# Performance work log

Hardware: AMD Instinct MI355X
Metric: run time of the kernel (lower is better)

Reference implementation:

```python
import jax, jax.numpy as jnp
import numpy as np

T, B, E, H = 256, 8, 512, 32
EXP = 512            # number of expanded (periodic-image) keys
SMOOTH = 20.0        # smooth_factor


def setup_inputs() -> dict:
    key = jax.random.key(0)
    ks = jax.random.split(key, 12)
    s = 1.0 / np.sqrt(E)
    return {
        "query": jax.random.normal(ks[0], (T, B, E), dtype=jnp.float32),
        "outcell_index": jax.random.randint(ks[1], (B, EXP), 0, T),
        "expand_mask": jax.random.bernoulli(ks[2], 0.1, (B, EXP)),
        "key_padding_mask": jax.random.bernoulli(ks[3], 0.1, (B, T)),
        "local_attention_weight": jax.random.uniform(ks[4], (B, T, T + EXP), dtype=jnp.float32),
        "Wq": jax.random.normal(ks[5], (E, E), dtype=jnp.float32) * s,
        "bq": jnp.zeros((E,), dtype=jnp.float32),
        "Wk": jax.random.normal(ks[6], (E, E), dtype=jnp.float32) * s,   # k_bias=False
        "Wv": jax.random.normal(ks[7], (E, E), dtype=jnp.float32) * s,
        "bv": jnp.zeros((E,), dtype=jnp.float32),
        "Wo": jax.random.normal(ks[8], (E, E), dtype=jnp.float32) * s,
        "bo": jnp.zeros((E,), dtype=jnp.float32),
    }


def reference(query, outcell_index, expand_mask, key_padding_mask,
              local_attention_weight, Wq, bq, Wk, Wv, bv, Wo, bo):
    t, b, e = query.shape
    hd = e // H
    # QKV projections (torch Linear: y = x @ W.T + b)
    q = jnp.einsum('tbe,fe->tbf', query, Wq) + bq
    k = jnp.einsum('tbe,fe->tbf', query, Wk)          # no k bias
    v = jnp.einsum('tbe,fe->tbf', query, Wv) + bv
    # PBC gather-expand K/V along the time axis
    oc = outcell_index.T[:, :, None]                  # [EXP, B, 1]
    k = jnp.concatenate([k, jnp.take_along_axis(k, oc, axis=0)], axis=0)  # [S,B,E]
    v = jnp.concatenate([v, jnp.take_along_axis(v, oc, axis=0)], axis=0)
    s_len = k.shape[0]
    # [len, B, E] -> [B, H, len, hd]
    qh = q.reshape(t, b, H, hd).transpose(1, 2, 0, 3)
    kh = k.reshape(s_len, b, H, hd).transpose(1, 2, 0, 3)
    vh = v.reshape(s_len, b, H, hd).transpose(1, 2, 0, 3)
    # NOTE: forward() never applies self.scaling in this path (faithful)
    scores = jnp.einsum('bhtd,bhsd->bhts', qh, kh)    # [B,H,T,S]
    law = local_attention_weight[:, None]             # [B,1,T,S]
    scores = (scores + SMOOTH) * law - SMOOTH         # smooth softmax
    kpm = jnp.concatenate([key_padding_mask, expand_mask], axis=1)  # [B,S]
    scores = jnp.where(kpm[:, None, None, :], -jnp.inf, scores)
    probs = jax.nn.softmax(scores, axis=-1)
    probs = probs * law                               # post-softmax reweight
    attn = jnp.einsum('bhts,bhsd->bhtd', probs, vh)   # [B,H,T,hd]
    attn = attn.transpose(2, 0, 1, 3).reshape(t, b, e)
    return jnp.einsum('tbe,fe->tbf', attn, Wo) + bo
```

## Files before the change

### kernel.cpp

```cpp
#include <hip/hip_runtime.h>
#include <stdint.h>

#define T_ 256
#define B_ 8
#define E_ 512
#define H_ 32
#define HD_ 16
#define EXP_ 512
#define S_ 768
#define M_ 2048
#define SMOOTH_ 20.0f
#define PSTR 40
#define VSTR 800
#define OSTR 20
#define LOG2E_ 1.44269504f
#define MB0_  (-100.988655f)

typedef __attribute__((ext_vector_type(8)))  short bf16x8;
typedef __attribute__((ext_vector_type(4)))  float f32x4;
typedef __attribute__((ext_vector_type(16))) float f32x16;

__device__ __forceinline__ unsigned int pku(float a, float b)
{
    return ((__float_as_uint(a) + 0x8000u) >> 16) |
           ((__float_as_uint(b) + 0x8000u) & 0xFFFF0000u);
}
__device__ __forceinline__ ushort bf1(float a)
{
    unsigned int u = __float_as_uint(a);
    u = u + 0x7FFFu + ((u >> 16) & 1u);
    return (ushort)(u >> 16);
}

union U16 { uint4 u; bf16x8 v; };

template<bool AF, bool BF>
__device__ __forceinline__ void gemm_body(const void* __restrict__ Xp, int xstep,
                                          const void* __restrict__ Wp, int wstep,
                                          f32x4 acc[2][2],
                                          ushort* As, ushort* Bs)
{
    const int tid  = threadIdx.x;
    const int lrow = tid >> 2;
    const int kq   = tid & 3;
    const int l    = tid & 63;
    const int w    = tid >> 6;
    const int wm   = w & 1;
    const int wn   = w >> 1;
    const int lq   = l >> 4;
    const int ln   = l & 15;

    ushort* Aw = &As[lrow * 72 + kq * 16];
    ushort* Bw = &Bs[lrow * 72 + kq * 16];

    const float*  Xf = (const float*)Xp;
    const ushort* Xh = (const ushort*)Xp;
    const float*  Wf = (const float*)Wp;
    const ushort* Wh = (const ushort*)Wp;

    float4 fa0, fa1, fa2, fa3, fb0, fb1, fb2, fb3;
    uint4  ha0, ha1, hb0, hb1;

    if (AF) {
        fa0 = *(const float4*)&Xf[0];  fa1 = *(const float4*)&Xf[4];
        fa2 = *(const float4*)&Xf[8];  fa3 = *(const float4*)&Xf[12];
    } else {
        ha0 = *(const uint4*)&Xh[0];   ha1 = *(const uint4*)&Xh[8];
    }
    if (BF) {
        fb0 = *(const float4*)&Wf[0];  fb1 = *(const float4*)&Wf[4];
        fb2 = *(const float4*)&Wf[8];  fb3 = *(const float4*)&Wf[12];
    } else {
        hb0 = *(const uint4*)&Wh[0];   hb1 = *(const uint4*)&Wh[8];
    }

    for (int it = 0; it < E_ / 64; ++it) {
        __syncthreads();
        if (AF) {
            *(uint4*)&Aw[0] = make_uint4(pku(fa0.x, fa0.y), pku(fa0.z, fa0.w),
                                         pku(fa1.x, fa1.y), pku(fa1.z, fa1.w));
            *(uint4*)&Aw[8] = make_uint4(pku(fa2.x, fa2.y), pku(fa2.z, fa2.w),
                                         pku(fa3.x, fa3.y), pku(fa3.z, fa3.w));
        } else {
            *(uint4*)&Aw[0] = ha0;
            *(uint4*)&Aw[8] = ha1;
        }
        if (BF) {
            *(uint4*)&Bw[0] = make_uint4(pku(fb0.x, fb0.y), pku(fb0.z, fb0.w),
                                         pku(fb1.x, fb1.y), pku(fb1.z, fb1.w));
            *(uint4*)&Bw[8] = make_uint4(pku(fb2.x, fb2.y), pku(fb2.z, fb2.w),
                                         pku(fb3.x, fb3.y), pku(fb3.z, fb3.w));
        } else {
            *(uint4*)&Bw[0] = hb0;
            *(uint4*)&Bw[8] = hb1;
        }
        __syncthreads();
        if (it < E_ / 64 - 1) {
            if (AF) {
                Xf += xstep;
                fa0 = *(const float4*)&Xf[0];  fa1 = *(const float4*)&Xf[4];
                fa2 = *(const float4*)&Xf[8];  fa3 = *(const float4*)&Xf[12];
            } else {
                Xh += xstep;
                ha0 = *(const uint4*)&Xh[0];   ha1 = *(const uint4*)&Xh[8];
            }
            if (BF) {
                Wf += wstep;
                fb0 = *(const float4*)&Wf[0];  fb1 = *(const float4*)&Wf[4];
                fb2 = *(const float4*)&Wf[8];  fb3 = *(const float4*)&Wf[12];
            } else {
                Wh += wstep;
                hb0 = *(const uint4*)&Wh[0];   hb1 = *(const uint4*)&Wh[8];
            }
        }
#pragma unroll
        for (int kb = 0; kb < 2; ++kb) {
            bf16x8 af0 = *(const bf16x8*)&As[(32 * wm + ln) * 72 + 32 * kb + lq * 8];
            bf16x8 af1 = *(const bf16x8*)&As[(32 * wm + 16 + ln) * 72 + 32 * kb + lq * 8];
            bf16x8 bf0 = *(const bf16x8*)&Bs[(32 * wn + ln) * 72 + 32 * kb + lq * 8];
            bf16x8 bf1 = *(const bf16x8*)&Bs[(32 * wn + 16 + ln) * 72 + 32 * kb + lq * 8];
            acc[0][0] = __builtin_amdgcn_mfma_f32_16x16x32_bf16(af0, bf0, acc[0][0], 0, 0, 0);
            acc[0][1] = __builtin_amdgcn_mfma_f32_16x16x32_bf16(af0, bf1, acc[0][1], 0, 0, 0);
            acc[1][0] = __builtin_amdgcn_mfma_f32_16x16x32_bf16(af1, bf0, acc[1][0], 0, 0, 0);
            acc[1][1] = __builtin_amdgcn_mfma_f32_16x16x32_bf16(af1, bf1, acc[1][1], 0, 0, 0);
        }
    }
}

__global__ __launch_bounds__(256)
void qkv_gemm(const float* __restrict__ X,
              const float* __restrict__ Wq, const float* __restrict__ Wk,
              const float* __restrict__ Wv,
              const float* __restrict__ bq, const float* __restrict__ bv,
              ushort* __restrict__ Qb, ushort* __restrict__ Kb,
              ushort* __restrict__ Vb)
{
    __shared__ __align__(16) ushort AsBs[2 * 64 * 72];
    ushort* As = AsBs;
    ushort* Bs = AsBs + 64 * 72;

    const int z = blockIdx.z;
    const float* W     = (z == 0) ? Wq : (z == 1 ? Wk : Wv);
    const float* bias  = (z == 0) ? bq : (z == 2 ? bv : nullptr);
    ushort* dst        = (z == 0) ? Qb : (z == 1 ? Kb : Vb);

    const int m0 = blockIdx.y * 64;
    const int n0 = blockIdx.x * 64;

    f32x4 acc[2][2];
#pragma unroll
    for (int i = 0; i < 2; ++i)
#pragma unroll
        for (int j = 0; j < 2; ++j)
            acc[i][j] = (f32x4){0.f, 0.f, 0.f, 0.f};

    const int tid  = threadIdx.x;
    const int lrow = tid >> 2;
    const int kq   = tid & 3;
    gemm_body<true, true>(&X[(size_t)(m0 + lrow) * E_ + kq * 16], 64,
                          &W[(size_t)(n0 + lrow) * E_ + kq * 16], 64,
                          acc, As, Bs);

    const int l  = tid & 63;
    const int w  = tid >> 6;
    const int wm = w & 1;
    const int wn = w >> 1;
    const int lq = l >> 4;
    const int ln = l & 15;

    const float b0_ = bias ? bias[n0 + 32 * wn + ln]      : 0.f;
    const float b1_ = bias ? bias[n0 + 32 * wn + 16 + ln] : 0.f;

    __syncthreads();
    ushort* Ls = As;
#pragma unroll
    for (int j = 0; j < 2; ++j) {
        const float bb = j ? b1_ : b0_;
#pragma unroll
        for (int i = 0; i < 2; ++i)
#pragma unroll
            for (int r = 0; r < 4; ++r)
                Ls[(32 * wm + 16 * i + lq * 4 + r) * 72 + 32 * wn + 16 * j + ln] =
                    bf1(acc[i][j][r] + bb);
    }
    __syncthreads();

    {
        const int lm = tid & 63;
        const int hh = tid >> 6;
        uint4 f0 = *(const uint4*)&Ls[lm * 72 + hh * 16];
        uint4 f1 = *(const uint4*)&Ls[lm * 72 + hh * 16 + 8];
        const int m = m0 + lm;
        const int t = m >> 3;
        const int b = m & 7;
        const int h = (n0 >> 4) + hh;
        ushort* dp = &dst[(((size_t)(b * H_ + h)) * T_ + t) * HD_];
        *(uint4*)&dp[0] = f0;
        *(uint4*)&dp[8] = f1;
    }
}

__global__ __launch_bounds__(256)
void out_gemm(const ushort* __restrict__ Ab, const float* __restrict__ Wo,
              const float* __restrict__ bo, float* __restrict__ dst)
{
    __shared__ __align__(16) ushort AsBs[2 * 64 * 72];
    ushort* As = AsBs;
    ushort* Bs = AsBs + 64 * 72;

    const int m0 = blockIdx.y * 64;
    const int n0 = blockIdx.x * 64;

    f32x4 acc[2][2];
#pragma unroll
    for (int i = 0; i < 2; ++i)
#pragma unroll
        for (int j = 0; j < 2; ++j)
            acc[i][j] = (f32x4){0.f, 0.f, 0.f, 0.f};

    const int tid  = threadIdx.x;
    const int lrow = tid >> 2;
    const int kq   = tid & 3;
    const int m    = m0 + lrow;
    const int t    = m >> 3;
    const int b    = m & 7;
    gemm_body<false, true>(&Ab[(((size_t)(b * H_ + kq)) * T_ + t) * HD_], 4 * T_ * HD_,
                           &Wo[(size_t)(n0 + lrow) * E_ + kq * 16], 64,
                           acc, As, Bs);

    const int l  = tid & 63;
    const int w  = tid >> 6;
    const int wm = w & 1;
    const int wn = w >> 1;
    const int lq = l >> 4;
    const int ln = l & 15;

    const float bo0 = bo[n0 + 32 * wn + ln];
    const float bo1 = bo[n0 + 32 * wn + 16 + ln];

    __syncthreads();
    float* Lf = (float*)AsBs;
#pragma unroll
    for (int j = 0; j < 2; ++j) {
        const float bb = j ? bo1 : bo0;
#pragma unroll
        for (int i = 0; i < 2; ++i)
#pragma unroll
            for (int r = 0; r < 4; ++r)
                Lf[(32 * wm + 16 * i + lq * 4 + r) * 68 + 32 * wn + 16 * j + ln] =
                    acc[i][j][r] + bb;
    }
    __syncthreads();

    {
        const int lm = tid & 63;
        const int hh = tid >> 6;
        float* dp = &dst[(size_t)(m0 + lm) * E_ + n0 + hh * 16];
#pragma unroll
        for (int c = 0; c < 4; ++c) {
            float4 v = *(const float4*)&Lf[lm * 68 + hh * 16 + c * 4];
            *(float4*)&dp[c * 4] = v;
        }
    }
}

__device__ __forceinline__ void scat8(ushort* d, uint4 u)
{
    d[0 * VSTR] = (ushort)(u.x);  d[1 * VSTR] = (ushort)(u.x >> 16);
    d[2 * VSTR] = (ushort)(u.y);  d[3 * VSTR] = (ushort)(u.y >> 16);
    d[4 * VSTR] = (ushort)(u.z);  d[5 * VSTR] = (ushort)(u.z >> 16);
    d[6 * VSTR] = (ushort)(u.w);  d[7 * VSTR] = (ushort)(u.w >> 16);
}

__global__ __launch_bounds__(512)
void attn_kernel(const ushort* __restrict__ Qb, const ushort* __restrict__ Kb,
                 const ushort* __restrict__ Vb, const float* __restrict__ LAW,
                 const int* __restrict__ kpm, const int* __restrict__ em,
                 const int* __restrict__ oc, ushort* __restrict__ Ab)
{
    __shared__ __align__(16) ushort Ks[S_ * HD_];
    __shared__ __align__(16) ushort Vt[HD_ * VSTR];
    __shared__ __align__(16) float  msf[S_];
    __shared__ __align__(16) ushort Pb[8][32 * PSTR];
    __shared__ __align__(16) float  Zpart[2][128];

    float*  Obuf = (float*)Ks;
    ushort* Ob   = (ushort*)Vt;

    const int tid    = threadIdx.x;
    const int blk    = blockIdx.x;
    const int bh     = blk >> 1;
    const int thalf  = blk & 1;
    const int b      = bh >> 5;
    const int h      = bh & 31;

    ((uint4*)Ks)[tid] = ((const uint4*)&Kb[(size_t)bh * T_ * HD_])[tid];
    {
        const int t    = tid >> 1;
        const int half = tid & 1;
        uint4 v = *(const uint4*)&Vb[((size_t)bh * T_ + t) * HD_ + half * 8];
        scat8(&Vt[half * 8 * VSTR + t], v);
    }
    {
        const int j   = tid;
        const int src = oc[b * EXP_ + j];
        const uint4* kr = (const uint4*)&Kb[((size_t)bh * T_ + src) * HD_];
        *(uint4*)&Ks[(T_ + j) * HD_ + 0] = kr[0];
        *(uint4*)&Ks[(T_ + j) * HD_ + 8] = kr[1];
        const uint4* vr = (const uint4*)&Vb[((size_t)bh * T_ + src) * HD_];
        scat8(&Vt[T_ + j], vr[0]);
        scat8(&Vt[8 * VSTR + T_ + j], vr[1]);
    }
    {
        const int s = tid;
        const int m = (s < T_) ? kpm[b * T_ + s] : em[b * EXP_ + (s - T_)];
        msf[s] = m ? -1.0e5f : MB0_;
        if (tid < 256) {
            const int s2 = 512 + tid;
            msf[s2] = em[b * EXP_ + (s2 - T_)] ? -1.0e5f : MB0_;
        }
    }

    const int w      = tid >> 6;
    const int l      = tid & 63;
    const int slane  = l & 31;
    const int khalf  = l >> 5;
    const int wt     = w & 3;
    const int sh     = w >> 2;
    const int tbase  = thalf * 128 + wt * 32;
    bf16x8 qf = *(const bf16x8*)&Qb[((size_t)bh * T_ + tbase + slane) * HD_ + khalf * 8];

    __syncthreads();

    const f32x16 zero16 = {0.f,0.f,0.f,0.f,0.f,0.f,0.f,0.f,
                           0.f,0.f,0.f,0.f,0.f,0.f,0.f,0.f};
    f32x4 o0 = {0.f, 0.f, 0.f, 0.f};
    f32x4 o1 = {0.f, 0.f, 0.f, 0.f};
    float zacc[16];
#pragma unroll
    for (int r = 0; r < 16; ++r) zacc[r] = 0.f;

    const float* lawb = &LAW[((size_t)b * T_ + tbase + khalf * 4) * S_ + slane];
    ushort* pw = &Pb[w][slane];
    const int tl = l & 15;
    const int kg = l >> 4;

    for (int i = sh * 12; i < sh * 12 + 12; ++i) {
        bf16x8 kf = *(const bf16x8*)&Ks[(i * 32 + slane) * HD_ + khalf * 8];

        float lw[16];
        const float* lp = lawb + i * 32;
#pragma unroll
        for (int r = 0; r < 16; ++r)
            lw[r] = lp[(size_t)((r & 3) + 8 * (r >> 2)) * S_];

        f32x16 sc = __builtin_amdgcn_mfma_f32_32x32x16_bf16(qf, kf, zero16, 0, 0, 0);
        const float mb = msf[i * 32 + slane];

#pragma unroll
        for (int r = 0; r < 16; ++r) {
            const float lwK = lw[r] * LOG2E_;
            const float arg = __builtin_fmaf(sc[r], lwK,
                              __builtin_fmaf(lwK, SMOOTH_, mb));
            const float e = __builtin_amdgcn_exp2f(arg);
            zacc[r] += e;
            const float p = e * lw[r];
            pw[((r & 3) + 8 * (r >> 2) + 4 * khalf) * PSTR] =
                (ushort)((__float_as_uint(p) + 0x8000u) >> 16);
        }

        bf16x8 vf = *(const bf16x8*)&Vt[tl * VSTR + i * 32 + kg * 8];
        {
            const ushort* pr0 = &Pb[w][(0 * 16 + tl) * PSTR + kg * 8];
            U16 u;
            uint2 a0 = *(const uint2*)pr0;
            uint2 a1 = *(const uint2*)(pr0 + 4);
            u.u = make_uint4(a0.x, a0.y, a1.x, a1.y);
            o0 = __builtin_amdgcn_mfma_f32_16x16x32_bf16(vf, u.v, o0, 0, 0, 0);
            const ushort* pr1 = &Pb[w][(1 * 16 + tl) * PSTR + kg * 8];
            uint2 b0 = *(const uint2*)pr1;
            uint2 b1 = *(const uint2*)(pr1 + 4);
            u.u = make_uint4(b0.x, b0.y, b1.x, b1.y);
            o1 = __builtin_amdgcn_mfma_f32_16x16x32_bf16(vf, u.v, o1, 0, 0, 0);
        }
    }

#pragma unroll
    for (int m = 1; m < 32; m <<= 1) {
#pragma unroll
        for (int r = 0; r < 16; ++r)
            zacc[r] += __shfl_xor(zacc[r], m);
    }

    __syncthreads();

    if (l == 0 || l == 32) {
#pragma unroll
        for (int r = 0; r < 16; ++r)
            Zpart[sh][wt * 32 + (r & 3) + 8 * (r >> 2) + 4 * khalf] = zacc[r];
    }
    if (sh == 1) {
#pragma unroll
        for (int th = 0; th < 2; ++th) {
            const f32x4 o = th ? o1 : o0;
            *(float4*)&Obuf[((wt * 2 + th) * 16 + tl) * OSTR + kg * 4] =
                make_float4(o[0], o[1], o[2], o[3]);
        }
    }
    __syncthreads();

    if (sh == 0) {
#pragma unroll
        for (int th = 0; th < 2; ++th) {
            const int trow = wt * 32 + th * 16 + tl;
            const float Zt  = Zpart[0][trow] + Zpart[1][trow];
            const float inv = (Zt > 0.f) ? 1.f / Zt : 0.f;
            float4 po = *(const float4*)&Obuf[((wt * 2 + th) * 16 + tl) * OSTR + kg * 4];
            const f32x4 o = th ? o1 : o0;
            float ov[4] = {(o[0] + po.x) * inv, (o[1] + po.y) * inv,
                           (o[2] + po.z) * inv, (o[3] + po.w) * inv};
            *(uint*)&Ob[trow * 16 + kg * 4]     = pku(ov[0], ov[1]);
            *(uint*)&Ob[trow * 16 + kg * 4 + 2] = pku(ov[2], ov[3]);
        }
    }
    __syncthreads();

    if (tid < 256) {
        ushort* dp = &Ab[(((size_t)(b * H_ + h)) * T_ + thalf * 128) * HD_];
        *(uint4*)&dp[tid * 8] = *(const uint4*)&Ob[tid * 8];
    }
}

extern "C" void kernel_launch(void* const* d_in, const int* in_sizes, int n_in,
                              void* d_out, int out_size, void* d_ws, size_t ws_size,
                              hipStream_t stream)
{
    const float* query = (const float*)d_in[0];
    const int*   oc    = (const int*)d_in[1];
    const int*   em    = (const int*)d_in[2];
    const int*   kpm   = (const int*)d_in[3];
    const float* law   = (const float*)d_in[4];
    const float* Wq    = (const float*)d_in[5];
    const float* bq    = (const float*)d_in[6];
    const float* Wk    = (const float*)d_in[7];
    const float* Wv    = (const float*)d_in[8];
    const float* bv    = (const float*)d_in[9];
    const float* Wo    = (const float*)d_in[10];
    const float* bo    = (const float*)d_in[11];
    float* out = (float*)d_out;

    ushort* Qb = (ushort*)d_ws;
    ushort* Kb = Qb + (size_t)1048576;
    ushort* Vb = Kb + (size_t)1048576;
    ushort* Ab = Vb + (size_t)1048576;

    dim3 gq(E_ / 64, M_ / 64, 3);
    qkv_gemm<<<gq, 256, 0, stream>>>(query, Wq, Wk, Wv, bq, bv, Qb, Kb, Vb);

    attn_kernel<<<B_ * H_ * 2, 512, 0, stream>>>(Qb, Kb, Vb, law, kpm, em, oc, Ab);

    dim3 go(E_ / 64, M_ / 64, 1);
    out_gemm<<<go, 256, 0, stream>>>(Ab, Wo, bo, out);
}
```

Measured before the change: 130.8 us.

## Fuse QKV projection into attention kernel, one block per batch-head

Replaces the separate QKV GEMM and attention kernels with one kernel in which each (batch, head) block computes its own 256x48 Q/K/V slice straight from fp32 input and weights into shared memory, then runs attention. This removes the Q/K/V global round trip and one launch, and the PBC gather becomes a shared-memory copy. In exchange the grid drops from 512 to 256 blocks, each block rereads the whole query batch slice (256x512 fp32), and large shared memory limits occupancy. Each block now walks all 24 key chunks instead of splitting them across two wave groups.

Measured after the change: 138.6 us. 1.06x slower.

```diff
diff --git a/kernel.cpp b/kernel.cpp
--- a/kernel.cpp
+++ b/kernel.cpp
@@ -12,7 +12,6 @@
 #define SMOOTH_ 20.0f
 #define PSTR 40
 #define VSTR 800
-#define OSTR 20
 #define LOG2E_ 1.44269504f
 #define MB0_  (-100.988655f)
 
@@ -33,6 +32,218 @@
 }
 
 union U16 { uint4 u; bf16x8 v; };
+
+__global__ __launch_bounds__(512)
+void qkv_attn_kernel(const float* __restrict__ X,
+                     const float* __restrict__ Wq, const float* __restrict__ Wk,
+                     const float* __restrict__ Wv,
+                     const float* __restrict__ bq, const float* __restrict__ bv,
+                     const float* __restrict__ LAW,
+                     const int* __restrict__ kpm, const int* __restrict__ em,
+                     const int* __restrict__ oc, ushort* __restrict__ Ab)
+{
+    __shared__ __align__(16) char raw[82944];
+    ushort* Ks  = (ushort*)(raw);
+    ushort* Vt  = (ushort*)(raw + 24576);
+    ushort* Qi  = (ushort*)(raw + 50176);
+    float*  msf = (float*) (raw + 58368);
+    ushort* Pbb = (ushort*)(raw + 61440);
+    float*  Zb  = (float*) (raw + 81920);
+    ushort* As  = (ushort*)(raw);
+    ushort* Bs  = (ushort*)(raw + 36864);
+    ushort* Ob  = Qi;
+
+    const int bh  = blockIdx.x;
+    const int b   = bh >> 5;
+    const int h   = bh & 31;
+    const int tid = threadIdx.x;
+    const int w   = tid >> 6;
+    const int l   = tid & 63;
+
+    const int lr = tid >> 1;
+    const int kq = tid & 1;
+    const float* Xr = &X[((size_t)lr * 8 + b) * E_ + kq * 32];
+    const int wr = tid >> 3;
+    const int wk = tid & 7;
+    const float* Wsel = (wr < 16) ? Wq : (wr < 32 ? Wk : Wv);
+    const float* Wr = &Wsel[((size_t)(h * 16 + (wr & 15))) * E_ + wk * 8];
+    const bool wload = (tid < 384);
+
+    ushort* Axw = &As[lr * 72 + kq * 32];
+    ushort* Bxw = &Bs[wr * 72 + wk * 8];
+
+    f32x4 acc[2][3];
+#pragma unroll
+    for (int i = 0; i < 2; ++i)
+#pragma unroll
+        for (int m = 0; m < 3; ++m)
+            acc[i][m] = (f32x4){0.f, 0.f, 0.f, 0.f};
+
+    float4 xp[8], wp[2];
+#pragma unroll
+    for (int j = 0; j < 8; ++j) xp[j] = *(const float4*)&Xr[j * 4];
+    if (wload) { wp[0] = *(const float4*)&Wr[0]; wp[1] = *(const float4*)&Wr[4]; }
+
+    const int ln = l & 15;
+    const int lg = l >> 4;
+
+    for (int it = 0; it < 8; ++it) {
+        __syncthreads();
+#pragma unroll
+        for (int g = 0; g < 4; ++g)
+            *(uint4*)&Axw[g * 8] = make_uint4(
+                pku(xp[2*g].x, xp[2*g].y),   pku(xp[2*g].z, xp[2*g].w),
+                pku(xp[2*g+1].x, xp[2*g+1].y), pku(xp[2*g+1].z, xp[2*g+1].w));
+        if (wload)
+            *(uint4*)&Bxw[0] = make_uint4(pku(wp[0].x, wp[0].y), pku(wp[0].z, wp[0].w),
+                                          pku(wp[1].x, wp[1].y), pku(wp[1].z, wp[1].w));
+        __syncthreads();
+        if (it < 7) {
+            Xr += 64;
+#pragma unroll
+            for (int j = 0; j < 8; ++j) xp[j] = *(const float4*)&Xr[j * 4];
+            if (wload) { Wr += 64; wp[0] = *(const float4*)&Wr[0]; wp[1] = *(const float4*)&Wr[4]; }
+        }
+#pragma unroll
+        for (int kb = 0; kb < 2; ++kb) {
+            bf16x8 af0 = *(const bf16x8*)&As[(32 * w + ln) * 72 + kb * 32 + lg * 8];
+            bf16x8 af1 = *(const bf16x8*)&As[(32 * w + 16 + ln) * 72 + kb * 32 + lg * 8];
+#pragma unroll
+            for (int m = 0; m < 3; ++m) {
+                bf16x8 bfm = *(const bf16x8*)&Bs[(m * 16 + ln) * 72 + kb * 32 + lg * 8];
+                acc[0][m] = __builtin_amdgcn_mfma_f32_16x16x32_bf16(af0, bfm, acc[0][m], 0, 0, 0);
+                acc[1][m] = __builtin_amdgcn_mfma_f32_16x16x32_bf16(af1, bfm, acc[1][m], 0, 0, 0);
+            }
+        }
+    }
+
+    __syncthreads();
+
+    {
+        const float bqv = bq[h * 16 + ln];
+        const float bvv = bv[h * 16 + ln];
+#pragma unroll
+        for (int i = 0; i < 2; ++i)
+#pragma unroll
+            for (int r = 0; r < 4; ++r) {
+                const int t = 32 * w + 16 * i + lg * 4 + r;
+                Qi[t * 16 + ln]    = bf1(acc[i][0][r] + bqv);
+                Ks[t * 16 + ln]    = bf1(acc[i][1][r]);
+                Vt[ln * VSTR + t]  = bf1(acc[i][2][r] + bvv);
+            }
+    }
+    __syncthreads();
+
+    {
+        const int j   = tid;
+        const int src = oc[b * EXP_ + j];
+        uint4 k0 = *(const uint4*)&Ks[src * 16];
+        uint4 k1 = *(const uint4*)&Ks[src * 16 + 8];
+        *(uint4*)&Ks[(T_ + j) * 16]     = k0;
+        *(uint4*)&Ks[(T_ + j) * 16 + 8] = k1;
+#pragma unroll
+        for (int d = 0; d < 16; ++d)
+            Vt[d * VSTR + T_ + j] = Vt[d * VSTR + src];
+
+        const int s = tid;
+        const int m = (s < T_) ? kpm[b * T_ + s] : em[b * EXP_ + (s - T_)];
+        msf[s] = m ? -1.0e5f : MB0_;
+        if (tid < 256) {
+            const int s2 = 512 + tid;
+            msf[s2] = em[b * EXP_ + (s2 - T_)] ? -1.0e5f : MB0_;
+        }
+    }
+    __syncthreads();
+
+    const int slane = l & 31;
+    const int khalf = l >> 5;
+    const int tl = l & 15;
+    const int kg = l >> 4;
+
+    bf16x8 qf = *(const bf16x8*)&Qi[(w * 32 + slane) * 16 + khalf * 8];
+
+    const f32x16 zero16 = {0.f,0.f,0.f,0.f,0.f,0.f,0.f,0.f,
+                           0.f,0.f,0.f,0.f,0.f,0.f,0.f,0.f};
+    f32x4 o0 = {0.f, 0.f, 0.f, 0.f};
+    f32x4 o1 = {0.f, 0.f, 0.f, 0.f};
+    float zacc[16];
+#pragma unroll
+    for (int r = 0; r < 16; ++r) zacc[r] = 0.f;
+
+    const float* lawb = &LAW[((size_t)b * T_ + w * 32 + khalf * 4) * S_ + slane];
+    ushort* pw = &Pbb[w * 32 * PSTR + slane];
+    ushort* pt = &Pbb[w * 32 * PSTR];
+
+    for (int i = 0; i < S_ / 32; ++i) {
+        bf16x8 kf = *(const bf16x8*)&Ks[(i * 32 + slane) * 16 + khalf * 8];
+
+        float lw[16];
+        const float* lp = lawb + i * 32;
+#pragma unroll
+        for (int r = 0; r < 16; ++r)
+            lw[r] = lp[(size_t)((r & 3) + 8 * (r >> 2)) * S_];
+
+        f32x16 sc = __builtin_amdgcn_mfma_f32_32x32x16_bf16(qf, kf, zero16, 0, 0, 0);
+        const float mb = msf[i * 32 + slane];
+
+#pragma unroll
+        for (int r = 0; r < 16; ++r) {
+            const float lwK = lw[r] * LOG2E_;
+            const float arg = __builtin_fmaf(sc[r], lwK,
+                              __builtin_fmaf(lwK, SMOOTH_, mb));
+            const float e = __builtin_amdgcn_exp2f(arg);
+            zacc[r] += e;
+            const float p = e * lw[r];
+            pw[((r & 3) + 8 * (r >> 2) + 4 * khalf) * PSTR] =
+                (ushort)((__float_as_uint(p) + 0x8000u) >> 16);
+        }
+
+        bf16x8 vf = *(const bf16x8*)&Vt[tl * VSTR + i * 32 + kg * 8];
+        {
+            const ushort* pr0 = &pt[(0 * 16 + tl) * PSTR + kg * 8];
+            U16 u;
+            uint2 a0 = *(const uint2*)pr0;
+            uint2 a1 = *(const uint2*)(pr0 + 4);
+            u.u = make_uint4(a0.x, a0.y, a1.x, a1.y);
+            o0 = __builtin_amdgcn_mfma_f32_16x16x32_bf16(vf, u.v, o0, 0, 0, 0);
+            const ushort* pr1 = &pt[(1 * 16 + tl) * PSTR + kg * 8];
+            uint2 b0 = *(const uint2*)pr1;
+            uint2 b1 = *(const uint2*)(pr1 + 4);
+            u.u = make_uint4(b0.x, b0.y, b1.x, b1.y);
+            o1 = __builtin_amdgcn_mfma_f32_16x16x32_bf16(vf, u.v, o1, 0, 0, 0);
+        }
+    }
+
+#pragma unroll
+    for (int m = 1; m < 32; m <<= 1) {
+#pragma unroll
+        for (int r = 0; r < 16; ++r)
+            zacc[r] += __shfl_xor(zacc[r], m);
+    }
+    if (l == 0 || l == 32) {
+#pragma unroll
+        for (int r = 0; r < 16; ++r)
+            Zb[w * 32 + (r & 3) + 8 * (r >> 2) + 4 * khalf] = zacc[r];
+    }
+    __syncthreads();
+
+#pragma unroll
+    for (int th = 0; th < 2; ++th) {
+        const int trow = th * 16 + tl;
+        const float Zt  = Zb[w * 32 + trow];
+        const float inv = (Zt > 0.f) ? 1.f / Zt : 0.f;
+        const f32x4 o = th ? o1 : o0;
+        const int t = w * 32 + trow;
+        *(uint*)&Ob[t * 16 + kg * 4]     = pku(o[0] * inv, o[1] * inv);
+        *(uint*)&Ob[t * 16 + kg * 4 + 2] = pku(o[2] * inv, o[3] * inv);
+    }
+    __syncthreads();
+
+    {
+        ushort* dp = &Ab[((size_t)(b * H_ + h)) * T_ * HD_];
+        *(uint4*)&dp[tid * 8] = *(const uint4*)&Ob[tid * 8];
+    }
+}
 
 template<bool AF, bool BF>
 __device__ __forceinline__ void gemm_body(const void* __restrict__ Xp, int xstep,
@@ -53,65 +264,34 @@
     ushort* Aw = &As[lrow * 72 + kq * 16];
     ushort* Bw = &Bs[lrow * 72 + kq * 16];
 
-    const float*  Xf = (const float*)Xp;
     const ushort* Xh = (const ushort*)Xp;
     const float*  Wf = (const float*)Wp;
-    const ushort* Wh = (const ushort*)Wp;
-
-    float4 fa0, fa1, fa2, fa3, fb0, fb1, fb2, fb3;
-    uint4  ha0, ha1, hb0, hb1;
-
-    if (AF) {
-        fa0 = *(const float4*)&Xf[0];  fa1 = *(const float4*)&Xf[4];
-        fa2 = *(const float4*)&Xf[8];  fa3 = *(const float4*)&Xf[12];
-    } else {
-        ha0 = *(const uint4*)&Xh[0];   ha1 = *(const uint4*)&Xh[8];
-    }
-    if (BF) {
-        fb0 = *(const float4*)&Wf[0];  fb1 = *(const float4*)&Wf[4];
-        fb2 = *(const float4*)&Wf[8];  fb3 = *(const float4*)&Wf[12];
-    } else {
-        hb0 = *(const uint4*)&Wh[0];   hb1 = *(const uint4*)&Wh[8];
-    }
+
+    uint4  ha0 = *(const uint4*)&Xh[0];
+    uint4  ha1 = *(const uint4*)&Xh[8];
+    float4 fb0 = *(const float4*)&Wf[0];
+    float4 fb1 = *(const float4*)&Wf[4];
+    float4 fb2 = *(const float4*)&Wf[8];
+    float4 fb3 = *(const float4*)&Wf[12];
 
     for (int it = 0; it < E_ / 64; ++it) {
         __syncthreads();
-        if (AF) {
-            *(uint4*)&Aw[0] = make_uint4(pku(fa0.x, fa0.y), pku(fa0.z, fa0.w),
-                                         pku(fa1.x, fa1.y), pku(fa1.z, fa1.w));
-            *(uint4*)&Aw[8] = make_uint4(pku(fa2.x, fa2.y), pku(fa2.z, fa2.w),
-                                         pku(fa3.x, fa3.y), pku(fa3.z, fa3.w));
-        } else {
-            *(uint4*)&Aw[0] = ha0;
-            *(uint4*)&Aw[8] = ha1;
-        }
-        if (BF) {
-            *(uint4*)&Bw[0] = make_uint4(pku(fb0.x, fb0.y), pku(fb0.z, fb0.w),
-                                         pku(fb1.x, fb1.y), pku(fb1.z, fb1.w));
-            *(uint4*)&Bw[8] = make_uint4(pku(fb2.x, fb2.y), pku(fb2.z, fb2.w),
-                                         pku(fb3.x, fb3.y), pku(fb3.z, fb3.w));
-        } else {
-            *(uint4*)&Bw[0] = hb0;
-            *(uint4*)&Bw[8] = hb1;
-        }
+        *(uint4*)&Aw[0] = ha0;
+        *(uint4*)&Aw[8] = ha1;
+        *(uint4*)&Bw[0] = make_uint4(pku(fb0.x, fb0.y), pku(fb0.z, fb0.w),
+                                     pku(fb1.x, fb1.y), pku(fb1.z, fb1.w));
+        *(uint4*)&Bw[8] = make_uint4(pku(fb2.x, fb2.y), pku(fb2.z, fb2.w),
+                                     pku(fb3.x, fb3.y), pku(fb3.z, fb3.w));
         __syncthreads();
         if (it < E_ / 64 - 1) {
-            if (AF) {
-                Xf += xstep;
-                fa0 = *(const float4*)&Xf[0];  fa1 = *(const float4*)&Xf[4];
-                fa2 = *(const float4*)&Xf[8];  fa3 = *(const float4*)&Xf[12];
-            } else {
-                Xh += xstep;
-                ha0 = *(const uint4*)&Xh[0];   ha1 = *(const uint4*)&Xh[8];
-            }
-            if (BF) {
-                Wf += wstep;
-                fb0 = *(const float4*)&Wf[0];  fb1 = *(const float4*)&Wf[4];
-                fb2 = *(const float4*)&Wf[8];  fb3 = *(const float4*)&Wf[12];
-            } else {
-                Wh += wstep;
-                hb0 = *(const uint4*)&Wh[0];   hb1 = *(const uint4*)&Wh[8];
-            }
+            Xh += xstep;
+            ha0 = *(const uint4*)&Xh[0];
+            ha1 = *(const uint4*)&Xh[8];
+            Wf += wstep;
+            fb0 = *(const float4*)&Wf[0];
+            fb1 = *(const float4*)&Wf[4];
+            fb2 = *(const float4*)&Wf[8];
+            fb3 = *(const float4*)&Wf[12];
         }
 #pragma unroll
         for (int kb = 0; kb < 2; ++kb) {
@@ -128,79 +308,6 @@
 }
 
 __global__ __launch_bounds__(256)
-void qkv_gemm(const float* __restrict__ X,
-              const float* __restrict__ Wq, const float* __restrict__ Wk,
-              const float* __restrict__ Wv,
-              const float* __restrict__ bq, const float* __restrict__ bv,
-              ushort* __restrict__ Qb, ushort* __restrict__ Kb,
-              ushort* __restrict__ Vb)
-{
-    __shared__ __align__(16) ushort AsBs[2 * 64 * 72];
-    ushort* As = AsBs;
-    ushort* Bs = AsBs + 64 * 72;
-
-    const int z = blockIdx.z;
-    const float* W     = (z == 0) ? Wq : (z == 1 ? Wk : Wv);
-    const float* bias  = (z == 0) ? bq : (z == 2 ? bv : nullptr);
-    ushort* dst        = (z == 0) ? Qb : (z == 1 ? Kb : Vb);
-
-    const int m0 = blockIdx.y * 64;
-    const int n0 = blockIdx.x * 64;
-
-    f32x4 acc[2][2];
-#pragma unroll
-    for (int i = 0; i < 2; ++i)
-#pragma unroll
-        for (int j = 0; j < 2; ++j)
-            acc[i][j] = (f32x4){0.f, 0.f, 0.f, 0.f};
-
-    const int tid  = threadIdx.x;
-    const int lrow = tid >> 2;
-    const int kq   = tid & 3;
-    gemm_body<true, true>(&X[(size_t)(m0 + lrow) * E_ + kq * 16], 64,
-                          &W[(size_t)(n0 + lrow) * E_ + kq * 16], 64,
-                          acc, As, Bs);
-
-    const int l  = tid & 63;
-    const int w  = tid >> 6;
-    const int wm = w & 1;
-    const int wn = w >> 1;
-    const int lq = l >> 4;
-    const int ln = l & 15;
-
-    const float b0_ = bias ? bias[n0 + 32 * wn + ln]      : 0.f;
-    const float b1_ = bias ? bias[n0 + 32 * wn + 16 + ln] : 0.f;
-
-    __syncthreads();
-    ushort* Ls = As;
-#pragma unroll
-    for (int j = 0; j < 2; ++j) {
-        const float bb = j ? b1_ : b0_;
-#pragma unroll
-        for (int i = 0; i < 2; ++i)
-#pragma unroll
-            for (int r = 0; r < 4; ++r)
-                Ls[(32 * wm + 16 * i + lq * 4 + r) * 72 + 32 * wn + 16 * j + ln] =
-                    bf1(acc[i][j][r] + bb);
-    }
-    __syncthreads();
-
-    {
-        const int lm = tid & 63;
-        const int hh = tid >> 6;
-        uint4 f0 = *(const uint4*)&Ls[lm * 72 + hh * 16];
-        uint4 f1 = *(const uint4*)&Ls[lm * 72 + hh * 16 + 8];
-        const int m = m0 + lm;
-        const int t = m >> 3;
-        const int b = m & 7;
-        const int h = (n0 >> 4) + hh;
-        ushort* dp = &dst[(((size_t)(b * H_ + h)) * T_ + t) * HD_];
-        *(uint4*)&dp[0] = f0;
-        *(uint4*)&dp[8] = f1;
-    }
-}
-
-__global__ __launch_bounds__(256)
 void out_gemm(const ushort* __restrict__ Ab, const float* __restrict__ Wo,
               const float* __restrict__ bo, float* __restrict__ dst)
 {
@@ -261,173 +368,6 @@
             float4 v = *(const float4*)&Lf[lm * 68 + hh * 16 + c * 4];
             *(float4*)&dp[c * 4] = v;
         }
-    }
-}
-
-__device__ __forceinline__ void scat8(ushort* d, uint4 u)
-{
-    d[0 * VSTR] = (ushort)(u.x);  d[1 * VSTR] = (ushort)(u.x >> 16);
-    d[2 * VSTR] = (ushort)(u.y);  d[3 * VSTR] = (ushort)(u.y >> 16);
-    d[4 * VSTR] = (ushort)(u.z);  d[5 * VSTR] = (ushort)(u.z >> 16);
-    d[6 * VSTR] = (ushort)(u.w);  d[7 * VSTR] = (ushort)(u.w >> 16);
-}
-
-__global__ __launch_bounds__(512)
-void attn_kernel(const ushort* __restrict__ Qb, const ushort* __restrict__ Kb,
-                 const ushort* __restrict__ Vb, const float* __restrict__ LAW,
-                 const int* __restrict__ kpm, const int* __restrict__ em,
-                 const int* __restrict__ oc, ushort* __restrict__ Ab)
-{
-    __shared__ __align__(16) ushort Ks[S_ * HD_];
-    __shared__ __align__(16) ushort Vt[HD_ * VSTR];
-    __shared__ __align__(16) float  msf[S_];
-    __shared__ __align__(16) ushort Pb[8][32 * PSTR];
-    __shared__ __align__(16) float  Zpart[2][128];
-
-    float*  Obuf = (float*)Ks;
-    ushort* Ob   = (ushort*)Vt;
-
-    const int tid    = threadIdx.x;
-    const int blk    = blockIdx.x;
-    const int bh     = blk >> 1;
-    const int thalf  = blk & 1;
-    const int b      = bh >> 5;
-    const int h      = bh & 31;
-
-    ((uint4*)Ks)[tid] = ((const uint4*)&Kb[(size_t)bh * T_ * HD_])[tid];
-    {
-        const int t    = tid >> 1;
-        const int half = tid & 1;
-        uint4 v = *(const uint4*)&Vb[((size_t)bh * T_ + t) * HD_ + half * 8];
-        scat8(&Vt[half * 8 * VSTR + t], v);
-    }
-    {
-        const int j   = tid;
-        const int src = oc[b * EXP_ + j];
-        const uint4* kr = (const uint4*)&Kb[((size_t)bh * T_ + src) * HD_];
-        *(uint4*)&Ks[(T_ + j) * HD_ + 0] = kr[0];
-        *(uint4*)&Ks[(T_ + j) * HD_ + 8] = kr[1];
-        const uint4* vr = (const uint4*)&Vb[((size_t)bh * T_ + src) * HD_];
-        scat8(&Vt[T_ + j], vr[0]);
-        scat8(&Vt[8 * VSTR + T_ + j], vr[1]);
-    }
-    {
-        const int s = tid;
-        const int m = (s < T_) ? kpm[b * T_ + s] : em[b * EXP_ + (s - T_)];
-        msf[s] = m ? -1.0e5f : MB0_;
-        if (tid < 256) {
-            const int s2 = 512 + tid;
-            msf[s2] = em[b * EXP_ + (s2 - T_)] ? -1.0e5f : MB0_;
-        }
-    }
-
-    const int w      = tid >> 6;
-    const int l      = tid & 63;
-    const int slane  = l & 31;
-    const int khalf  = l >> 5;
-    const int wt     = w & 3;
-    const int sh     = w >> 2;
-    const int tbase  = thalf * 128 + wt * 32;
-    bf16x8 qf = *(const bf16x8*)&Qb[((size_t)bh * T_ + tbase + slane) * HD_ + khalf * 8];
-
-    __syncthreads();
-
-    const f32x16 zero16 = {0.f,0.f,0.f,0.f,0.f,0.f,0.f,0.f,
-                           0.f,0.f,0.f,0.f,0.f,0.f,0.f,0.f};
-    f32x4 o0 = {0.f, 0.f, 0.f, 0.f};
-    f32x4 o1 = {0.f, 0.f, 0.f, 0.f};
-    float zacc[16];
-#pragma unroll
-    for (int r = 0; r < 16; ++r) zacc[r] = 0.f;
-
-    const float* lawb = &LAW[((size_t)b * T_ + tbase + khalf * 4) * S_ + slane];
-    ushort* pw = &Pb[w][slane];
-    const int tl = l & 15;
-    const int kg = l >> 4;
-
-    for (int i = sh * 12; i < sh * 12 + 12; ++i) {
-        bf16x8 kf = *(const bf16x8*)&Ks[(i * 32 + slane) * HD_ + khalf * 8];
-
-        float lw[16];
-        const float* lp = lawb + i * 32;
-#pragma unroll
-        for (int r = 0; r < 16; ++r)
-            lw[r] = lp[(size_t)((r & 3) + 8 * (r >> 2)) * S_];
-
-        f32x16 sc = __builtin_amdgcn_mfma_f32_32x32x16_bf16(qf, kf, zero16, 0, 0, 0);
-        const float mb = msf[i * 32 + slane];
-
-#pragma unroll
-        for (int r = 0; r < 16; ++r) {
-            const float lwK = lw[r] * LOG2E_;
-            const float arg = __builtin_fmaf(sc[r], lwK,
-                              __builtin_fmaf(lwK, SMOOTH_, mb));
-            const float e = __builtin_amdgcn_exp2f(arg);
-            zacc[r] += e;
-            const float p = e * lw[r];
-            pw[((r & 3) + 8 * (r >> 2) + 4 * khalf) * PSTR] =
-                (ushort)((__float_as_uint(p) + 0x8000u) >> 16);
-        }
-
-        bf16x8 vf = *(const bf16x8*)&Vt[tl * VSTR + i * 32 + kg * 8];
-        {
-            const ushort* pr0 = &Pb[w][(0 * 16 + tl) * PSTR + kg * 8];
-            U16 u;
-            uint2 a0 = *(const uint2*)pr0;
-            uint2 a1 = *(const uint2*)(pr0 + 4);
-            u.u = make_uint4(a0.x, a0.y, a1.x, a1.y);
-            o0 = __builtin_amdgcn_mfma_f32_16x16x32_bf16(vf, u.v, o0, 0, 0, 0);
-            const ushort* pr1 = &Pb[w][(1 * 16 + tl) * PSTR + kg * 8];
-            uint2 b0 = *(const uint2*)pr1;
-            uint2 b1 = *(const uint2*)(pr1 + 4);
-            u.u = make_uint4(b0.x, b0.y, b1.x, b1.y);
-            o1 = __builtin_amdgcn_mfma_f32_16x16x32_bf16(vf, u.v, o1, 0, 0, 0);
-        }
-    }
-
-#pragma unroll
-    for (int m = 1; m < 32; m <<= 1) {
-#pragma unroll
-        for (int r = 0; r < 16; ++r)
-            zacc[r] += __shfl_xor(zacc[r], m);
-    }
-
-    __syncthreads();
-
-    if (l == 0 || l == 32) {
-#pragma unroll
-        for (int r = 0; r < 16; ++r)
-            Zpart[sh][wt * 32 + (r & 3) + 8 * (r >> 2) + 4 * khalf] = zacc[r];
-    }
-    if (sh == 1) {
-#pragma unroll
-        for (int th = 0; th < 2; ++th) {
-            const f32x4 o = th ? o1 : o0;
-            *(float4*)&Obuf[((wt * 2 + th) * 16 + tl) * OSTR + kg * 4] =
-                make_float4(o[0], o[1], o[2], o[3]);
-        }
-    }
-    __syncthreads();
-
-    if (sh == 0) {
-#pragma unroll
-        for (int th = 0; th < 2; ++th) {
-            const int trow = wt * 32 + th * 16 + tl;
-            const float Zt  = Zpart[0][trow] + Zpart[1][trow];
-            const float inv = (Zt > 0.f) ? 1.f / Zt : 0.f;
-            float4 po = *(const float4*)&Obuf[((wt * 2 + th) * 16 + tl) * OSTR + kg * 4];
-            const f32x4 o = th ? o1 : o0;
-            float ov[4] = {(o[0] + po.x) * inv, (o[1] + po.y) * inv,
-                           (o[2] + po.z) * inv, (o[3] + po.w) * inv};
-            *(uint*)&Ob[trow * 16 + kg * 4]     = pku(ov[0], ov[1]);
-            *(uint*)&Ob[trow * 16 + kg * 4 + 2] = pku(ov[2], ov[3]);
-        }
-    }
-    __syncthreads();
-
-    if (tid < 256) {
-        ushort* dp = &Ab[(((size_t)(b * H_ + h)) * T_ + thalf * 128) * HD_];
-        *(uint4*)&dp[tid * 8] = *(const uint4*)&Ob[tid * 8];
     }
 }
 
@@ -449,15 +389,10 @@
     const float* bo    = (const float*)d_in[11];
     float* out = (float*)d_out;
 
-    ushort* Qb = (ushort*)d_ws;
-    ushort* Kb = Qb + (size_t)1048576;
-    ushort* Vb = Kb + (size_t)1048576;
-    ushort* Ab = Vb + (size_t)1048576;
-
-    dim3 gq(E_ / 64, M_ / 64, 3);
-    qkv_gemm<<<gq, 256, 0, stream>>>(query, Wq, Wk, Wv, bq, bv, Qb, Kb, Vb);
-
-    attn_kernel<<<B_ * H_ * 2, 512, 0, stream>>>(Qb, Kb, Vb, law, kpm, em, oc, Ab);
+    ushort* Ab = (ushort*)d_ws;
+
+    qkv_attn_kernel<<<B_ * H_, 512, 0, stream>>>(query, Wq, Wk, Wv, bq, bv,
+                                                 law, kpm, em, oc, Ab);
 
     dim3 go(E_ / 64, M_ / 64, 1);
     out_gemm<<<go, 256, 0, stream>>>(Ab, Wo, bo, out);
```
